# Optimization experiments

Hardware: AMD Instinct MI355X
Metric: run time of the kernel (lower is better)

The kernel has to match this reference:

```python
import jax, jax.numpy as jnp
from jax import lax
import numpy as np


def setup_inputs() -> dict:
    key = jax.random.key(0)
    kx, = jax.random.split(key, 1)
    B, T = 4096, 4096
    x = jax.random.normal(kx, (B, T), dtype=jnp.float32)
    omega_log = jnp.asarray(0.0, dtype=jnp.float32)
    alpha_log = jnp.asarray(0.0, dtype=jnp.float32)
    beta_log = jnp.asarray(0.0, dtype=jnp.float32)
    return {"x": x, "omega_log": omega_log, "alpha_log": alpha_log, "beta_log": beta_log}


def reference(x, omega_log, alpha_log, beta_log):
    # x: [B, T]
    ea = jnp.exp(alpha_log)
    eb = jnp.exp(beta_log)
    denom = 1.0 + ea + eb
    omega = jnp.exp(omega_log)
    alpha = ea / denom
    beta = eb / denom

    # initial variance: unbiased sample variance over time (torch.var default ddof=1)
    s0 = jnp.var(x, axis=1, ddof=1)  # [B]

    xsq = jnp.swapaxes(x[:, :-1] ** 2, 0, 1)  # [T-1, B]

    def step(s_prev, x2_t):
        s_t = omega + alpha * x2_t + beta * s_prev
        return s_t, s_t

    _, rest = lax.scan(step, s0, xsq)  # rest: [T-1, B]
    sigma2 = jnp.concatenate([s0[None, :], rest], axis=0)  # [T, B]
    return jnp.sqrt(jnp.swapaxes(sigma2, 0, 1))  # [B, T]
```

## Files before the change

### kernel.cpp

```cpp
#include <hip/hip_runtime.h>
#include <math.h>

#define B_ROWS 4096
#define T_COLS 4096
#define NTHREADS 256
#define WPB (NTHREADS / 64)
#define NBLOCKS (B_ROWS / WPB)

__device__ __forceinline__ float rfl(float v) {
    return __int_as_float(__builtin_amdgcn_readfirstlane(__float_as_int(v)));
}

#define STEP(z, xv) fmaf(beta, (z), fmaf(alpha, (xv) * (xv), omega))
#define SQ(z) __builtin_amdgcn_sqrtf(z)

__global__ __launch_bounds__(NTHREADS, 4) void garch_fused(
    const float* __restrict__ x,
    const float* __restrict__ p_omega_log,
    const float* __restrict__ p_alpha_log,
    const float* __restrict__ p_beta_log,
    float* __restrict__ out)
{
    const int lane = threadIdx.x & 63;
    const int wv   = threadIdx.x >> 6;
    const long row = (long)blockIdx.x * WPB + wv;

    const float4* xr4 = reinterpret_cast<const float4*>(x + row * T_COLS) + lane * 16;
    float xs[64];
#pragma unroll
    for (int j = 0; j < 16; ++j)
        *reinterpret_cast<float4*>(&xs[4 * j]) = xr4[j];

    float ea_p  = expf(p_alpha_log[0]);
    float eb_p  = expf(p_beta_log[0]);
    float denom = 1.0f + ea_p + eb_p;
    float omega = rfl(expf(p_omega_log[0]));
    float alpha = rfl(ea_p / denom);
    float beta  = rfl(eb_p / denom);
    float beta2  = beta * beta;
    float beta4  = beta2 * beta2;
    float beta8  = beta4 * beta4;
    float beta16 = beta8 * beta8;
    float beta32 = beta16 * beta16;
    float beta31 = beta16 * beta8 * beta4 * beta2 * beta;

    float a0 = 0, a1 = 0, a2 = 0, a3 = 0, q0 = 0, q1 = 0, q2 = 0, q3 = 0;
#pragma unroll
    for (int k = 0; k < 64; k += 4) {
        a0 += xs[k + 0]; q0 = fmaf(xs[k + 0], xs[k + 0], q0);
        a1 += xs[k + 1]; q1 = fmaf(xs[k + 1], xs[k + 1], q1);
        a2 += xs[k + 2]; q2 = fmaf(xs[k + 2], xs[k + 2], q2);
        a3 += xs[k + 3]; q3 = fmaf(xs[k + 3], xs[k + 3], q3);
    }
    float s1 = (a0 + a1) + (a2 + a3);
    float s2 = (q0 + q1) + (q2 + q3);

    float prev = __shfl_up(xs[63], 1);

    float zA = (lane > 0) ? fmaf(alpha, prev * prev, omega) : 0.0f;
    float zB = 0.0f;
#pragma unroll
    for (int k = 0; k < 31; ++k) {
        zA = STEP(zA, xs[k]);
        zB = STEP(zB, xs[k + 31]);
    }
    zB = STEP(zB, xs[62]);
    float aA = (lane == 0) ? beta31 : beta32;
    float ib = fmaf(beta32, zA, zB);
    float ia = aA * beta32;

#pragma unroll
    for (int d = 32; d > 0; d >>= 1) {
        s1 += __shfl_xor(s1, d);
        s2 += __shfl_xor(s2, d);
    }
    float s0 = (s2 - s1 * s1 * (1.0f / T_COLS)) * (1.0f / (T_COLS - 1));
    s0 = fmaxf(s0, 0.0f);

#pragma unroll
    for (int d = 1; d < 64; d <<= 1) {
        float pa = __shfl_up(ia, d);
        float pb = __shfl_up(ib, d);
        if (lane >= d) { ib = fmaf(ia, pb, ib); ia = ia * pa; }
    }

    float pea = __shfl_up(ia, 1);
    float peb = __shfl_up(ib, 1);
    if (lane == 0) { pea = 1.0f; peb = 0.0f; }
    float eA = fmaf(pea, s0, peb);
    float eB = fmaf(aA, eA, zA);

    float4* orow4 = reinterpret_cast<float4*>(out + row * T_COLS) + lane * 16;

    {
        float z;
        float4 q;
        if (lane == 0) { z = eA; }
        else           { z = fmaf(beta, eA, fmaf(alpha, prev * prev, omega)); }
        q.x = SQ(z);
        z = STEP(z, xs[0]); q.y = SQ(z);
        z = STEP(z, xs[1]); q.z = SQ(z);
        z = STEP(z, xs[2]); q.w = SQ(z);
        orow4[0] = q;
#pragma unroll
        for (int j = 1; j < 8; ++j) {
            z = STEP(z, xs[4 * j - 1]); q.x = SQ(z);
            z = STEP(z, xs[4 * j + 0]); q.y = SQ(z);
            z = STEP(z, xs[4 * j + 1]); q.z = SQ(z);
            z = STEP(z, xs[4 * j + 2]); q.w = SQ(z);
            orow4[j] = q;
        }
    }
    {
        float z = eB;
        float4 q;
#pragma unroll
        for (int j = 8; j < 16; ++j) {
            z = STEP(z, xs[4 * j - 1]); q.x = SQ(z);
            z = STEP(z, xs[4 * j + 0]); q.y = SQ(z);
            z = STEP(z, xs[4 * j + 1]); q.z = SQ(z);
            z = STEP(z, xs[4 * j + 2]); q.w = SQ(z);
            orow4[j] = q;
        }
    }
}

extern "C" void kernel_launch(void* const* d_in, const int* in_sizes, int n_in,
                              void* d_out, int out_size, void* d_ws, size_t ws_size,
                              hipStream_t stream) {
    const float* x         = (const float*)d_in[0];
    const float* omega_log = (const float*)d_in[1];
    const float* alpha_log = (const float*)d_in[2];
    const float* beta_log  = (const float*)d_in[3];
    float* out = (float*)d_out;

    garch_fused<<<NBLOCKS, NTHREADS, 0, stream>>>(x, omega_log, alpha_log, beta_log, out);
}
```

Baseline: 129.4 us.

## Stream x twice from global instead of holding 64 floats in registers

```diff
diff --git a/kernel.cpp b/kernel.cpp
--- a/kernel.cpp
+++ b/kernel.cpp
@@ -26,10 +26,6 @@
     const long row = (long)blockIdx.x * WPB + wv;
 
     const float4* xr4 = reinterpret_cast<const float4*>(x + row * T_COLS) + lane * 16;
-    float xs[64];
-#pragma unroll
-    for (int j = 0; j < 16; ++j)
-        *reinterpret_cast<float4*>(&xs[4 * j]) = xr4[j];
 
     float ea_p  = expf(p_alpha_log[0]);
     float eb_p  = expf(p_beta_log[0]);
@@ -44,30 +40,39 @@
     float beta32 = beta16 * beta16;
     float beta31 = beta16 * beta8 * beta4 * beta2 * beta;
 
-    float a0 = 0, a1 = 0, a2 = 0, a3 = 0, q0 = 0, q1 = 0, q2 = 0, q3 = 0;
+    float sum0 = 0.0f, sum1 = 0.0f, ssq0 = 0.0f, ssq1 = 0.0f;
+    float zA = 0.0f, zB = 0.0f;
+    float x31, x63;
 #pragma unroll
-    for (int k = 0; k < 64; k += 4) {
-        a0 += xs[k + 0]; q0 = fmaf(xs[k + 0], xs[k + 0], q0);
-        a1 += xs[k + 1]; q1 = fmaf(xs[k + 1], xs[k + 1], q1);
-        a2 += xs[k + 2]; q2 = fmaf(xs[k + 2], xs[k + 2], q2);
-        a3 += xs[k + 3]; q3 = fmaf(xs[k + 3], xs[k + 3], q3);
+    for (int r = 0; r < 8; ++r) {
+        float4 a = xr4[r];
+        float4 b = xr4[r + 8];
+        sum0 += (a.x + a.y) + (a.z + a.w);
+        sum1 += (b.x + b.y) + (b.z + b.w);
+        ssq0 = fmaf(a.x, a.x, ssq0); ssq0 = fmaf(a.y, a.y, ssq0);
+        ssq0 = fmaf(a.z, a.z, ssq0); ssq0 = fmaf(a.w, a.w, ssq0);
+        ssq1 = fmaf(b.x, b.x, ssq1); ssq1 = fmaf(b.y, b.y, ssq1);
+        ssq1 = fmaf(b.z, b.z, ssq1); ssq1 = fmaf(b.w, b.w, ssq1);
+        if (r < 7) {
+            zA = STEP(zA, a.x); zA = STEP(zA, a.y); zA = STEP(zA, a.z); zA = STEP(zA, a.w);
+            zB = STEP(zB, b.x); zB = STEP(zB, b.y); zB = STEP(zB, b.z); zB = STEP(zB, b.w);
+        } else {
+            zA = STEP(zA, a.x); zA = STEP(zA, a.y); zA = STEP(zA, a.z); x31 = a.w;
+            zB = STEP(zB, b.x); zB = STEP(zB, b.y); zB = STEP(zB, b.z); x63 = b.w;
+        }
     }
-    float s1 = (a0 + a1) + (a2 + a3);
-    float s2 = (q0 + q1) + (q2 + q3);
+    float s1 = sum0 + sum1;
+    float s2 = ssq0 + ssq1;
 
-    float prev = __shfl_up(xs[63], 1);
+    float prev = __shfl_up(x63, 1);
+    float u = fmaf(alpha, prev * prev, omega);
+    float v = fmaf(alpha, x31 * x31, omega);
 
-    float zA = (lane > 0) ? fmaf(alpha, prev * prev, omega) : 0.0f;
-    float zB = 0.0f;
-#pragma unroll
-    for (int k = 0; k < 31; ++k) {
-        zA = STEP(zA, xs[k]);
-        zB = STEP(zB, xs[k + 31]);
-    }
-    zB = STEP(zB, xs[62]);
     float aA = (lane == 0) ? beta31 : beta32;
-    float ib = fmaf(beta32, zA, zB);
+    float bA = (lane == 0) ? zA : fmaf(beta31, u, zA);
+
     float ia = aA * beta32;
+    float ib = fmaf(beta32, bA, fmaf(beta31, v, zB));
 
 #pragma unroll
     for (int d = 32; d > 0; d >>= 1) {
@@ -88,40 +93,36 @@
     float peb = __shfl_up(ib, 1);
     if (lane == 0) { pea = 1.0f; peb = 0.0f; }
     float eA = fmaf(pea, s0, peb);
-    float eB = fmaf(aA, eA, zA);
+    float eB = fmaf(aA, eA, bA);
 
     float4* orow4 = reinterpret_cast<float4*>(out + row * T_COLS) + lane * 16;
 
-    {
-        float z;
-        float4 q;
-        if (lane == 0) { z = eA; }
-        else           { z = fmaf(beta, eA, fmaf(alpha, prev * prev, omega)); }
-        q.x = SQ(z);
-        z = STEP(z, xs[0]); q.y = SQ(z);
-        z = STEP(z, xs[1]); q.z = SQ(z);
-        z = STEP(z, xs[2]); q.w = SQ(z);
-        orow4[0] = q;
+    float zc = eA, zd = eB;
+    float carryA = prev;
+    float carryB = x31;
 #pragma unroll
-        for (int j = 1; j < 8; ++j) {
-            z = STEP(z, xs[4 * j - 1]); q.x = SQ(z);
-            z = STEP(z, xs[4 * j + 0]); q.y = SQ(z);
-            z = STEP(z, xs[4 * j + 1]); q.z = SQ(z);
-            z = STEP(z, xs[4 * j + 2]); q.w = SQ(z);
-            orow4[j] = q;
+    for (int j = 0; j < 8; ++j) {
+        float4 a = xr4[j];
+        float4 b = xr4[j + 8];
+        float4 qa, qb;
+
+        if (j == 0 && lane == 0) {
+        } else {
+            zc = STEP(zc, carryA);
         }
-    }
-    {
-        float z = eB;
-        float4 q;
-#pragma unroll
-        for (int j = 8; j < 16; ++j) {
-            z = STEP(z, xs[4 * j - 1]); q.x = SQ(z);
-            z = STEP(z, xs[4 * j + 0]); q.y = SQ(z);
-            z = STEP(z, xs[4 * j + 1]); q.z = SQ(z);
-            z = STEP(z, xs[4 * j + 2]); q.w = SQ(z);
-            orow4[j] = q;
-        }
+        qa.x = SQ(zc);
+        zd = STEP(zd, carryB);  qb.x = SQ(zd);
+        zc = STEP(zc, a.x);     qa.y = SQ(zc);
+        zd = STEP(zd, b.x);     qb.y = SQ(zd);
+        zc = STEP(zc, a.y);     qa.z = SQ(zc);
+        zd = STEP(zd, b.y);     qb.z = SQ(zd);
+        zc = STEP(zc, a.z);     qa.w = SQ(zc);
+        zd = STEP(zd, b.z);     qb.w = SQ(zd);
+        carryA = a.w;
+        carryB = b.w;
+
+        orow4[j]     = qa;
+        orow4[j + 8] = qb;
     }
 }
 
```

Result: slower. 154.5 us (+19.5%).
